# Kernel optimization log

Hardware: AMD Instinct MI355X
Metric: run time of the kernel (lower is better)

## Reference

```python
import jax, jax.numpy as jnp
import numpy as np

# ---- static config (matches init_kwargs) ----
N_NODES = 100_000; N_GRAPHS = 100; NPG = 1000; GRID = 32  # ceil(sqrt(1000))
N_EDGES = 1_600_000
IN_DIM = 64; POS_DIM = 16; HID = 16; HEADS = 4; HD = HID * HEADS  # 64
OUT_DIM = 10; DIV_WEIGHT = 0.1; BN_EPS = 1e-5; NEG_SLOPE = 0.2


def _segment_softmax(e, dst, n):
    emax = jax.ops.segment_max(e, dst, num_segments=n)
    p = jnp.exp(e - emax[dst])
    denom = jax.ops.segment_sum(p, dst, num_segments=n)
    return p / (denom[dst] + 1e-16)


def _gat(x, src, dst, n, W, a_src, a_dst, extra=None):
    """GATv1-style conv: per-head linear, additive attention, segment softmax over dst."""
    H, D = a_src.shape
    h = (x @ W).reshape(n, H, D)          # [N,H,D]
    s = (h * a_src).sum(-1)               # [N,H]
    d = (h * a_dst).sum(-1)               # [N,H]
    e = s[src] + d[dst]
    if extra is not None:
        e = e + extra                     # positional attention bias [E,H]
    e = jax.nn.leaky_relu(e, NEG_SLOPE)
    alpha = _segment_softmax(e, dst, n)   # [E,H]
    out = jax.ops.segment_sum(alpha[:, :, None] * h[src], dst, num_segments=n)
    return out.reshape(n, H * D)


def _div_loss(W):
    # head-diversity / orthogonality regularizer on per-head weight slices
    in_dim = W.shape[0]
    Wh = W.reshape(in_dim, HEADS, HID).transpose(1, 0, 2).reshape(HEADS, -1)
    Wn = Wh / (jnp.linalg.norm(Wh, axis=-1, keepdims=True) + 1e-12)
    G = Wn @ Wn.T
    off = G - jnp.eye(HEADS, dtype=W.dtype)
    return DIV_WEIGHT * (off ** 2).sum() / (HEADS * (HEADS - 1))


def _grid_pos(n, dtype):
    # normalized grid positions per graph (equal-size graphs of NPG nodes)
    i = jnp.arange(n) % NPG
    return jnp.stack([(i // GRID) / (GRID - 1), (i % GRID) / (GRID - 1)], -1).astype(dtype)


def _forward(x, edge_index, batch,
             pe_W, pe_b,
             l0_pW, l0_pas, l0_pad, l0_posW, l0_posb, l0_dW, l0_das, l0_dad, l0_fW, l0_fb, l0_g, l0_b,
             l1_pW, l1_pas, l1_pad, l1_posW, l1_posb, l1_dW, l1_das, l1_dad, l1_fW, l1_fb, l1_g, l1_b,
             res_W, res_b, task_W, task_b):
    n = x.shape[0]
    src, dst = edge_index[0], edge_index[1]
    pos = _grid_pos(n, x.dtype)
    rel = pos[dst] - pos[src]             # [E,2]
    h = jnp.concatenate([x, pos @ pe_W + pe_b], -1)  # positional encoding concat [N,80]

    def layer(h_in, pW, pas, pad, posW, posb, dW, das, dad, fW, fb, g, b):
        pos_out = _gat(h_in, src, dst, n, pW, pas, pad, extra=rel @ posW + posb)
        div_out = _gat(h_in, src, dst, n, dW, das, dad)
        fused = jnp.concatenate([pos_out, div_out], -1) @ fW + fb
        mu = fused.mean(0)
        var = fused.var(0)
        bn = (fused - mu) / jnp.sqrt(var + BN_EPS) * g + b
        return jax.nn.elu(bn), _div_loss(dW)

    h1, dl0 = layer(h, l0_pW, l0_pas, l0_pad, l0_posW, l0_posb, l0_dW, l0_das, l0_dad, l0_fW, l0_fb, l0_g, l0_b)
    h2, dl1 = layer(h1, l1_pW, l1_pas, l1_pad, l1_posW, l1_posb, l1_dW, l1_das, l1_dad, l1_fW, l1_fb, l1_g, l1_b)
    h2 = h2 + (h1 @ res_W + res_b)        # residual on layer >0

    pooled = jax.ops.segment_sum(h2, batch, num_segments=N_GRAPHS) / NPG  # mean pool
    task = pooled @ task_W + task_b       # [N_GRAPHS, OUT_DIM]
    return task, dl0 + dl1


def setup_inputs() -> dict:
    key = jax.random.key(0)
    keys = iter(jax.random.split(key, 64))
    nk = lambda: next(keys)
    w = lambda shape: jax.random.normal(nk(), shape, jnp.float32) * 0.05
    x = jax.random.normal(nk(), (N_NODES, IN_DIM), jnp.float32)
    gid = jnp.repeat(jnp.arange(N_GRAPHS), N_EDGES // N_GRAPHS)
    src = gid * NPG + jax.random.randint(nk(), (N_EDGES,), 0, NPG)
    dst = gid * NPG + jax.random.randint(nk(), (N_EDGES,), 0, NPG)
    edge_index = jnp.stack([src, dst]).astype(jnp.int32)
    batch = jnp.repeat(jnp.arange(N_GRAPHS), NPG).astype(jnp.int32)
    IN0 = IN_DIM + POS_DIM
    inp = dict(x=x, edge_index=edge_index, batch=batch,
               pe_W=w((2, POS_DIM)), pe_b=jnp.zeros((POS_DIM,), jnp.float32))
    for pref, din in (('l0', IN0), ('l1', HD)):
        inp[pref + '_pW'] = w((din, HD)); inp[pref + '_pas'] = w((HEADS, HID)); inp[pref + '_pad'] = w((HEADS, HID))
        inp[pref + '_posW'] = w((2, HEADS)); inp[pref + '_posb'] = jnp.zeros((HEADS,), jnp.float32)
        inp[pref + '_dW'] = w((din, HD)); inp[pref + '_das'] = w((HEADS, HID)); inp[pref + '_dad'] = w((HEADS, HID))
        inp[pref + '_fW'] = w((2 * HD, HD)); inp[pref + '_fb'] = jnp.zeros((HD,), jnp.float32)
        inp[pref + '_g'] = jnp.ones((HD,), jnp.float32); inp[pref + '_b'] = jnp.zeros((HD,), jnp.float32)
    inp['res_W'] = w((HD, HD)); inp['res_b'] = jnp.zeros((HD,), jnp.float32)
    inp['task_W'] = w((HD, OUT_DIM)); inp['task_b'] = jnp.zeros((OUT_DIM,), jnp.float32)
    return inp


def reference(x, edge_index, batch,
              pe_W, pe_b,
              l0_pW, l0_pas, l0_pad, l0_posW, l0_posb, l0_dW, l0_das, l0_dad, l0_fW, l0_fb, l0_g, l0_b,
              l1_pW, l1_pas, l1_pad, l1_posW, l1_posb, l1_dW, l1_das, l1_dad, l1_fW, l1_fb, l1_g, l1_b,
              res_W, res_b, task_W, task_b):
    return _forward(x, edge_index, batch, pe_W, pe_b,
                    l0_pW, l0_pas, l0_pad, l0_posW, l0_posb, l0_dW, l0_das, l0_dad, l0_fW, l0_fb, l0_g, l0_b,
                    l1_pW, l1_pas, l1_pad, l1_posW, l1_posb, l1_dW, l1_das, l1_dad, l1_fW, l1_fb, l1_g, l1_b,
                    res_W, res_b, task_W, task_b)
```

## Files before the change

### kernel.cpp

```cpp
#include <hip/hip_runtime.h>
#include <math.h>

#define N_NODES   100000
#define N_GRAPHS  100
#define NPG       1000
#define N_EDGES   1600000
#define EPG       16000
#define HID       16
#define HEADS     4
#define HD        64
#define OUT_DIM   10
#define BN_EPS    1e-5f
#define NEG_SLOPE 0.2f

#define LDA 68
#define GEMM_BLOCKS_C 1563

static const size_t OFF_SPART = 0;
static const size_t OFF_PEWS  = 7000000;
static const size_t OFF_STAT1 = 7001000;
static const size_t OFF_WFRAG = 7010000;
static const size_t OFF_WF2   = 7020000;
static const size_t OFF_POOL  = 7100000;
static const size_t OFF_HL    = 8000000;
static const size_t OFF_CAT   = 20800000;
static const size_t OFF_F0    = 33600000;
static const size_t OFF_F1    = 40000000;
static const size_t OFF_SPSP  = 46400000;
static const size_t OFF_SPSD  = 46800000;
static const size_t OFF_DPD   = 47200000;
static const size_t OFF_STATS = 48000000;
static const size_t OFF_CSR   = 48000128;
static const size_t OFF_SRT   = 48100144;

__device__ inline unsigned bf_pack(float x, float y) {
    unsigned ux = __float_as_uint(x);
    unsigned uy = __float_as_uint(y);
    ux = (ux + 0x7FFFu + ((ux >> 16) & 1u)) >> 16;
    uy = ((uy + 0x7FFFu + ((uy >> 16) & 1u)) >> 16) << 16;
    return ux | uy;
}
__device__ inline float bf_lo(unsigned u) { return __uint_as_float(u << 16); }
__device__ inline float bf_hi(unsigned u) { return __uint_as_float(u & 0xFFFF0000u); }

typedef __attribute__((ext_vector_type(8))) short bf16x8;
typedef __attribute__((ext_vector_type(4))) float f32x4;

__device__ inline bf16x8 frag_from(unsigned a, unsigned b, unsigned c, unsigned d) {
    uint4 u{a, b, c, d};
    return *reinterpret_cast<bf16x8*>(&u);
}

__global__ __launch_bounds__(1024) void sort_edges(const int* __restrict__ ei,
                                                   int* __restrict__ csr_off,
                                                   int* __restrict__ sorted_src) {
    __shared__ int hist[1024];
    __shared__ int scan[1024];
    const int g = blockIdx.x;
    const int t = threadIdx.x;
    const int* src = ei;
    const int* dst = ei + N_EDGES;
    const int e0 = g * EPG;
    const int nbase = g * NPG;

    hist[t] = 0;
    __syncthreads();
    for (int i = t; i < EPG; i += 1024) {
        int d = dst[e0 + i] - nbase;
        atomicAdd(&hist[d], 1);
    }
    __syncthreads();
    scan[t] = hist[t];
    __syncthreads();
    for (int off = 1; off < 1024; off <<= 1) {
        int v = (t >= off) ? scan[t - off] : 0;
        __syncthreads();
        scan[t] += v;
        __syncthreads();
    }
    int excl = scan[t] - hist[t];
    if (t < NPG) csr_off[nbase + t] = e0 + excl;
    if (g == 0 && t == 0) csr_off[N_NODES] = N_EDGES;
    __syncthreads();
    hist[t] = excl;
    __syncthreads();
    for (int i = t; i < EPG; i += 1024) {
        int s = src[e0 + i];
        int d = dst[e0 + i] - nbase;
        int slot = atomicAdd(&hist[d], 1);
        sorted_src[e0 + slot] = s;
    }
}

__global__ __launch_bounds__(256) void prep_all(const float* __restrict__ peW, const float* __restrict__ peb,
                                                const float* __restrict__ pW0, const float* __restrict__ dW0,
                                                const float* __restrict__ pW1, const float* __restrict__ dW1,
                                                const float* __restrict__ fW0, const float* __restrict__ fW1,
                                                float* __restrict__ pe,
                                                uint4* __restrict__ wfA,
                                                uint4* __restrict__ wfD,
                                                float* __restrict__ pool2,
                                                float* __restrict__ stats0,
                                                float* __restrict__ stats1) {
    const int t = threadIdx.x;
    const int b = blockIdx.x;
    if (b == 0) {
        if (t < 128) {
            int r = t >> 6, c = t & 63;
            float sp = 0.f, sd = 0.f;
            for (int m = 0; m < 16; ++m) {
                sp += peW[r * 16 + m] * pW0[(64 + m) * 64 + c];
                sd += peW[r * 16 + m] * dW0[(64 + m) * 64 + c];
            }
            pe[r * 64 + c] = sp;
            pe[192 + r * 64 + c] = sd;
        } else if (t < 192) {
            int c = t & 63;
            float sp = 0.f, sd = 0.f;
            for (int m = 0; m < 16; ++m) {
                sp += peb[m] * pW0[(64 + m) * 64 + c];
                sd += peb[m] * dW0[(64 + m) * 64 + c];
            }
            pe[128 + c] = sp;
            pe[320 + c] = sd;
        }
    } else if (b == 1) {
        for (int i = t; i < 2 * 4 * 4 * 64; i += 256) {
            const int lane  = i & 63;
            const int ct    = (i >> 6) & 3;
            const int kk    = (i >> 8) & 3;
            const int layer = i >> 10;
            const float* W = layer ? fW1 : fW0;
            const int col = ct * 16 + (lane & 15);
            const int kb  = kk * 32 + (lane >> 4) * 8;
            uint4 u;
            u.x = bf_pack(W[(kb + 0) * 64 + col], W[(kb + 1) * 64 + col]);
            u.y = bf_pack(W[(kb + 2) * 64 + col], W[(kb + 3) * 64 + col]);
            u.z = bf_pack(W[(kb + 4) * 64 + col], W[(kb + 5) * 64 + col]);
            u.w = bf_pack(W[(kb + 6) * 64 + col], W[(kb + 7) * 64 + col]);
            wfA[i] = u;
        }
    } else if (b == 2) {
        for (int i = t; i < 2048; i += 256) {
            const int lane  = i & 63;
            const int ct    = (i >> 6) & 3;
            const int kk    = (i >> 8) & 1;
            const int mat   = (i >> 9) & 1;
            const int layer = i >> 10;
            const float* W = layer ? (mat ? dW1 : pW1) : (mat ? dW0 : pW0);
            const int col = ct * 16 + (lane & 15);
            const int kb  = kk * 32 + (lane >> 4) * 8;
            uint4 u;
            u.x = bf_pack(W[(kb + 0) * 64 + col], W[(kb + 1) * 64 + col]);
            u.y = bf_pack(W[(kb + 2) * 64 + col], W[(kb + 3) * 64 + col]);
            u.z = bf_pack(W[(kb + 4) * 64 + col], W[(kb + 5) * 64 + col]);
            u.w = bf_pack(W[(kb + 6) * 64 + col], W[(kb + 7) * 64 + col]);
            wfD[i] = u;
        }
    } else {
        for (int i = t; i < 2 * N_GRAPHS * 64; i += 256) pool2[i] = 0.f;
        if (t < 128) { stats0[t] = 0.f; stats1[t] = 0.f; }
    }
}

__global__ __launch_bounds__(128) void reduce_stats(const float* __restrict__ part,
                                                    float* __restrict__ stats) {
    const int c = threadIdx.x;
    const int nb = GEMM_BLOCKS_C;
    const int per = (nb + gridDim.x - 1) / gridDim.x;
    const int b0 = blockIdx.x * per;
    int b1 = b0 + per; if (b1 > nb) b1 = nb;
    float s = 0.f;
    for (int b = b0; b < b1; ++b) s += part[(size_t)b * 128 + c];
    atomicAdd(&stats[c], s);
}

template <bool PE, bool BN>
__global__ __launch_bounds__(256) void gemm_dual_mfma(const float* __restrict__ A,
                                                      const unsigned* __restrict__ wf2,
                                                      const float* __restrict__ pe,
                                                      const float* __restrict__ pas,
                                                      const float* __restrict__ pad_,
                                                      const float* __restrict__ das,
                                                      const float* __restrict__ dad,
                                                      const float* __restrict__ posW,
                                                      const float* __restrict__ posb,
                                                      const float* __restrict__ stats,
                                                      const float* __restrict__ gamma,
                                                      const float* __restrict__ beta,
                                                      float* __restrict__ poolF,
                                                      unsigned* __restrict__ hl,
                                                      float* __restrict__ sps_p,
                                                      float* __restrict__ sps_d,
                                                      float2* __restrict__ dpd) {
    __shared__ float sD[4 * 2 * 16 * LDA];
    const int t = threadIdx.x;
    const int w = t >> 6, lane = t & 63;
    const int cidx = lane & 15, khi = lane >> 4;
    const int node0 = blockIdx.x * 64;

    bf16x8 wf[2][2][4];
#pragma unroll
    for (int mat = 0; mat < 2; ++mat)
#pragma unroll
        for (int kk = 0; kk < 2; ++kk)
#pragma unroll
            for (int ct = 0; ct < 4; ++ct)
                wf[mat][kk][ct] = *reinterpret_cast<const bf16x8*>(
                    wf2 + (size_t)((((mat * 2 + kk) * 4 + ct) * 64) + lane) * 4);

    const int node0w = node0 + w * 16;
    int gn = node0w + cidx; if (gn > N_NODES - 1) gn = N_NODES - 1;
    const float* ar = A + (size_t)gn * 64;
    bf16x8 ah[2], al[2];
#pragma unroll
    for (int kk = 0; kk < 2; ++kk) {
        const int k0 = kk * 32 + khi * 8;
        float4 f0 = *reinterpret_cast<const float4*>(ar + k0);
        float4 f1 = *reinterpret_cast<const float4*>(ar + k0 + 4);
        if (BN) {
            const float invN = 1.0f / (float)N_NODES;
            float4 sa = *reinterpret_cast<const float4*>(&stats[k0]);
            float4 sb = *reinterpret_cast<const float4*>(&stats[k0 + 4]);
            float4 qa = *reinterpret_cast<const float4*>(&stats[64 + k0]);
            float4 qb = *reinterpret_cast<const float4*>(&stats[64 + k0 + 4]);
            float4 ga = *reinterpret_cast<const float4*>(&gamma[k0]);
            float4 gb = *reinterpret_cast<const float4*>(&gamma[k0 + 4]);
            float4 ba = *reinterpret_cast<const float4*>(&beta[k0]);
            float4 bb = *reinterpret_cast<const float4*>(&beta[k0 + 4]);
            float sc[8], sh[8];
            float ss[8] = {sa.x, sa.y, sa.z, sa.w, sb.x, sb.y, sb.z, sb.w};
            float qq[8] = {qa.x, qa.y, qa.z, qa.w, qb.x, qb.y, qb.z, qb.w};
            float gg[8] = {ga.x, ga.y, ga.z, ga.w, gb.x, gb.y, gb.z, gb.w};
            float bt[8] = {ba.x, ba.y, ba.z, ba.w, bb.x, bb.y, bb.z, bb.w};
#pragma unroll
            for (int i = 0; i < 8; ++i) {
                float mu = ss[i] * invN;
                float var = qq[i] * invN - mu * mu;
                float iv = rsqrtf(var + BN_EPS);
                sc[i] = iv * gg[i];
                sh[i] = bt[i] - mu * sc[i];
            }
            auto ap = [&](float v, int i) {
                float r = fmaf(v, sc[i], sh[i]);
                return r > 0.f ? r : (__expf(r) - 1.f);
            };
            f0.x = ap(f0.x, 0); f0.y = ap(f0.y, 1); f0.z = ap(f0.z, 2); f0.w = ap(f0.w, 3);
            f1.x = ap(f1.x, 4); f1.y = ap(f1.y, 5); f1.z = ap(f1.z, 6); f1.w = ap(f1.w, 7);
            if (node0w < N_NODES) {
                const int node_l = node0w + cidx;
                const bool okn = node_l < N_NODES;
                const int gl = node_l / NPG;
                const int g0 = node0w / NPG;
                int lastn = node0w + 15; if (lastn > N_NODES - 1) lastn = N_NODES - 1;
                const int g1 = lastn / NPG;
                float p8[8] = {f0.x, f0.y, f0.z, f0.w, f1.x, f1.y, f1.z, f1.w};
                {
                    const bool m = okn && (gl == g0);
#pragma unroll
                    for (int i = 0; i < 8; ++i) {
                        float tv = m ? p8[i] : 0.f;
                        tv += __shfl_xor(tv, 1); tv += __shfl_xor(tv, 2);
                        tv += __shfl_xor(tv, 4); tv += __shfl_xor(tv, 8);
                        if (cidx == 0) atomicAdd(&poolF[g0 * 64 + k0 + i], tv);
                    }
                }
                if (g1 != g0) {
                    const bool m = okn && (gl == g1);
#pragma unroll
                    for (int i = 0; i < 8; ++i) {
                        float tv = m ? p8[i] : 0.f;
                        tv += __shfl_xor(tv, 1); tv += __shfl_xor(tv, 2);
                        tv += __shfl_xor(tv, 4); tv += __shfl_xor(tv, 8);
                        if (cidx == 0) atomicAdd(&poolF[g1 * 64 + k0 + i], tv);
                    }
                }
            }
        }
        unsigned h0 = bf_pack(f0.x, f0.y), h1 = bf_pack(f0.z, f0.w);
        unsigned h2 = bf_pack(f1.x, f1.y), h3 = bf_pack(f1.z, f1.w);
        unsigned l0 = bf_pack(f0.x - bf_lo(h0), f0.y - bf_hi(h0));
        unsigned l1 = bf_pack(f0.z - bf_lo(h1), f0.w - bf_hi(h1));
        unsigned l2 = bf_pack(f1.x - bf_lo(h2), f1.y - bf_hi(h2));
        unsigned l3 = bf_pack(f1.z - bf_lo(h3), f1.w - bf_hi(h3));
        ah[kk] = frag_from(h0, h1, h2, h3);
        al[kk] = frag_from(l0, l1, l2, l3);
    }

    f32x4 ap4[4], ad4[4];
#pragma unroll
    for (int ct = 0; ct < 4; ++ct) { ap4[ct] = 0.f; ad4[ct] = 0.f; }
#pragma unroll
    for (int ct = 0; ct < 4; ++ct) {
        ap4[ct] = __builtin_amdgcn_mfma_f32_16x16x32_bf16(ah[0], wf[0][0][ct], ap4[ct], 0, 0, 0);
        ap4[ct] = __builtin_amdgcn_mfma_f32_16x16x32_bf16(ah[1], wf[0][1][ct], ap4[ct], 0, 0, 0);
        ap4[ct] = __builtin_amdgcn_mfma_f32_16x16x32_bf16(al[0], wf[0][0][ct], ap4[ct], 0, 0, 0);
        ap4[ct] = __builtin_amdgcn_mfma_f32_16x16x32_bf16(al[1], wf[0][1][ct], ap4[ct], 0, 0, 0);
        ad4[ct] = __builtin_amdgcn_mfma_f32_16x16x32_bf16(ah[0], wf[1][0][ct], ad4[ct], 0, 0, 0);
        ad4[ct] = __builtin_amdgcn_mfma_f32_16x16x32_bf16(ah[1], wf[1][1][ct], ad4[ct], 0, 0, 0);
        ad4[ct] = __builtin_amdgcn_mfma_f32_16x16x32_bf16(al[0], wf[1][0][ct], ad4[ct], 0, 0, 0);
        ad4[ct] = __builtin_amdgcn_mfma_f32_16x16x32_bf16(al[1], wf[1][1][ct], ad4[ct], 0, 0, 0);
    }

    {
        float* base = sD + w * (2 * 16 * LDA);
#pragma unroll
        for (int ct = 0; ct < 4; ++ct)
#pragma unroll
            for (int q = 0; q < 4; ++q) {
                base[(khi * 4 + q) * LDA + ct * 16 + cidx]                 = ap4[ct][q];
                base[16 * LDA + (khi * 4 + q) * LDA + ct * 16 + cidx]      = ad4[ct][q];
            }
    }
    __syncthreads();

    const int tx = t & 15, ty = t >> 4;
    const int c4 = tx * 4;
    float4 accp[4], accd[4];
#pragma unroll
    for (int j = 0; j < 4; ++j) {
        const int n = ty * 4 + j;
        const float* bp = sD + (n >> 4) * (2 * 16 * LDA) + (n & 15) * LDA;
        accp[j] = *reinterpret_cast<const float4*>(bp + c4);
        accd[j] = *reinterpret_cast<const float4*>(bp + 16 * LDA + c4);
    }

    if (PE) {
        float4 pp0 = *reinterpret_cast<const float4*>(&pe[c4]);
        float4 pp1 = *reinterpret_cast<const float4*>(&pe[64 + c4]);
        float4 ppb = *reinterpret_cast<const float4*>(&pe[128 + c4]);
        float4 pd0 = *reinterpret_cast<const float4*>(&pe[192 + c4]);
        float4 pd1 = *reinterpret_cast<const float4*>(&pe[256 + c4]);
        float4 pdb = *reinterpret_cast<const float4*>(&pe[320 + c4]);
#pragma unroll
        for (int j = 0; j < 4; ++j) {
            int node = node0 + ty * 4 + j;
            int r = node % NPG;
            float px = (float)(r >> 5) * (1.0f / 31.0f);
            float py = (float)(r & 31) * (1.0f / 31.0f);
            accp[j].x += px * pp0.x + py * pp1.x + ppb.x;
            accp[j].y += px * pp0.y + py * pp1.y + ppb.y;
            accp[j].z += px * pp0.z + py * pp1.z + ppb.z;
            accp[j].w += px * pp0.w + py * pp1.w + ppb.w;
            accd[j].x += px * pd0.x + py * pd1.x + pdb.x;
            accd[j].y += px * pd0.y + py * pd1.y + pdb.y;
            accd[j].z += px * pd0.z + py * pd1.z + pdb.z;
            accd[j].w += px * pd0.w + py * pd1.w + pdb.w;
        }
    }

    float4 pasv = *reinterpret_cast<const float4*>(&pas[c4]);
    float4 padv = *reinterpret_cast<const float4*>(&pad_[c4]);
    float4 dasv = *reinterpret_cast<const float4*>(&das[c4]);
    float4 dadv = *reinterpret_cast<const float4*>(&dad[c4]);
    const int h = tx >> 2;
    const float pw0 = posW[h], pw1 = posW[4 + h], pb = posb[h];
    const int cu = tx * 2;
#pragma unroll
    for (int j = 0; j < 4; ++j) {
        const int node = node0 + ty * 4 + j;
        float vps = accp[j].x * pasv.x + accp[j].y * pasv.y + accp[j].z * pasv.z + accp[j].w * pasv.w;
        float vpd = accp[j].x * padv.x + accp[j].y * padv.y + accp[j].z * padv.z + accp[j].w * padv.w;
        float vds = accd[j].x * dasv.x + accd[j].y * dasv.y + accd[j].z * dasv.z + accd[j].w * dasv.w;
        float vdd = accd[j].x * dadv.x + accd[j].y * dadv.y + accd[j].z * dadv.z + accd[j].w * dadv.w;
        vps += __shfl_xor(vps, 1); vps += __shfl_xor(vps, 2);
        vpd += __shfl_xor(vpd, 1); vpd += __shfl_xor(vpd, 2);
        vds += __shfl_xor(vds, 1); vds += __shfl_xor(vds, 2);
        vdd += __shfl_xor(vdd, 1); vdd += __shfl_xor(vdd, 2);
        if (node < N_NODES) {
            uint2 up, ud;
            up.x = bf_pack(accp[j].x, accp[j].y); up.y = bf_pack(accp[j].z, accp[j].w);
            ud.x = bf_pack(accd[j].x, accd[j].y); ud.y = bf_pack(accd[j].z, accd[j].w);
            *reinterpret_cast<uint2*>(&hl[(size_t)node * 64 + cu])      = up;
            *reinterpret_cast<uint2*>(&hl[(size_t)node * 64 + 32 + cu]) = ud;
            if ((tx & 3) == 0) {
                const int r = node % NPG;
                const float pxn = (float)(r >> 5) * (1.0f / 31.0f);
                const float pyn = (float)(r & 31) * (1.0f / 31.0f);
                const float posdot = pxn * pw0 + pyn * pw1;
                sps_p[node * 4 + h] = vps - posdot;
                sps_d[node * 4 + h] = vds;
                dpd[node * 4 + h] = float2{vpd + posdot + pb, vdd};
            }
        }
    }
}

__global__ __launch_bounds__(256) void gemm_mfma_bf(const unsigned* __restrict__ A,
                                                    const unsigned* __restrict__ wfrag,
                                                    const float* __restrict__ bias,
                                                    float* __restrict__ out,
                                                    float* __restrict__ spart) {
    __shared__ float red[512];
    const int t = threadIdx.x;
    const int lane = t & 63;
    const int cidx = lane & 15;
    const int khi  = lane >> 4;

    bf16x8 wf[4][4];
#pragma unroll
    for (int kk = 0; kk < 4; ++kk)
#pragma unroll
        for (int ct = 0; ct < 4; ++ct)
            wf[kk][ct] = *reinterpret_cast<const bf16x8*>(wfrag + (size_t)((kk * 4 + ct) * 64 + lane) * 4);

    float bias_r[4];
#pragma unroll
    for (int ct = 0; ct < 4; ++ct) bias_r[ct] = bias[ct * 16 + cidx];

    float ls[4] = {0.f, 0.f, 0.f, 0.f};
    float lq[4] = {0.f, 0.f, 0.f, 0.f};

    const int NW  = gridDim.x << 2;
    const int wid = (blockIdx.x << 2) + (t >> 6);
    for (int tile = wid; tile < N_NODES / 16; tile += NW) {
        const int node0 = tile << 4;
        const unsigned* arow = A + (size_t)(node0 + cidx) * 64 + khi * 4;
        bf16x8 a0 = *reinterpret_cast<const bf16x8*>(arow);
        bf16x8 a1 = *reinterpret_cast<const bf16x8*>(arow + 16);
        bf16x8 a2 = *reinterpret_cast<const bf16x8*>(arow + 32);
        bf16x8 a3 = *reinterpret_cast<const bf16x8*>(arow + 48);

        f32x4 acc[4];
#pragma unroll
        for (int ct = 0; ct < 4; ++ct) acc[ct] = 0.f;
#pragma unroll
        for (int ct = 0; ct < 4; ++ct) {
            acc[ct] = __builtin_amdgcn_mfma_f32_16x16x32_bf16(a0, wf[0][ct], acc[ct], 0, 0, 0);
            acc[ct] = __builtin_amdgcn_mfma_f32_16x16x32_bf16(a1, wf[1][ct], acc[ct], 0, 0, 0);
            acc[ct] = __builtin_amdgcn_mfma_f32_16x16x32_bf16(a2, wf[2][ct], acc[ct], 0, 0, 0);
            acc[ct] = __builtin_amdgcn_mfma_f32_16x16x32_bf16(a3, wf[3][ct], acc[ct], 0, 0, 0);
        }

        const int nbase = node0 + (khi << 2);
#pragma unroll
        for (int ct = 0; ct < 4; ++ct) {
#pragma unroll
            for (int q = 0; q < 4; ++q) {
                float v = acc[ct][q] + bias_r[ct];
                out[(size_t)(nbase + q) * 64 + ct * 16 + cidx] = v;
                ls[ct] += v;
                lq[ct] = fmaf(v, v, lq[ct]);
            }
        }
    }

#pragma unroll
    for (int ct = 0; ct < 4; ++ct) {
        ls[ct] += __shfl_xor(ls[ct], 16); ls[ct] += __shfl_xor(ls[ct], 32);
        lq[ct] += __shfl_xor(lq[ct], 16); lq[ct] += __shfl_xor(lq[ct], 32);
    }
    if (lane < 16) {
        const int w = t >> 6;
#pragma unroll
        for (int ct = 0; ct < 4; ++ct) {
            red[w * 64 + ct * 16 + lane]       = ls[ct];
            red[256 + w * 64 + ct * 16 + lane] = lq[ct];
        }
    }
    __syncthreads();
    if (t < 64) {
        float s  = red[t] + red[64 + t] + red[128 + t] + red[192 + t];
        float sq = red[256 + t] + red[320 + t] + red[384 + t] + red[448 + t];
        spart[(size_t)blockIdx.x * 128 + t]      = s;
        spart[(size_t)blockIdx.x * 128 + 64 + t] = sq;
    }
}

__global__ __launch_bounds__(256) void gat_fused(const unsigned* __restrict__ hl,
                                                 const float* __restrict__ sps_p,
                                                 const float* __restrict__ sps_d,
                                                 const float2* __restrict__ dpd,
                                                 const int* __restrict__ csr_off,
                                                 const int* __restrict__ sorted_src,
                                                 unsigned* __restrict__ gat_cat) {
    const int b = blockIdx.x;
    const int logical = (b & 7) * 3125 + (b >> 3);
    const int v = logical * 4 + (threadIdx.x >> 6);
    if (v >= N_NODES) return;
    const int lane = threadIdx.x & 63;
    const int j1 = lane >> 3;
    const int p1 = (lane >> 2) & 1;
    const int h1 = lane & 3;
    const int phneed = ((lane >> 5) << 2) | ((lane & 31) >> 3);

    const float* __restrict__ spl = p1 ? sps_d : sps_p;
    const float2 dv1 = dpd[(size_t)v * 4 + h1];
    const float dval1 = p1 ? dv1.y : dv1.x;

    const int beg = __builtin_amdgcn_readfirstlane(csr_off[v]);
    const int end = __builtin_amdgcn_readfirstlane(csr_off[v + 1]);

    float2 acc = {0.f, 0.f};
    float wpart = 0.f;
    int e = beg;
    const int nfull = (end - beg) >> 3;

    int sA = 0, sB = 0;
    float svA = 0.f, svB = 0.f;
    if (nfull >= 1) { sA = sorted_src[e + j1]; svA = spl[(size_t)sA * 4 + h1]; }
    if (nfull >= 2) { sB = sorted_src[e + 8 + j1]; }

    for (int k = 0; k < nfull; ++k, e += 8) {
        int sC = 0;
        if (k + 2 < nfull) sC = sorted_src[e + 16 + j1];
        if (k + 1 < nfull) svB = spl[(size_t)sB * 4 + h1];
        float elog = svA + dval1;
        elog = fmaxf(elog, NEG_SLOPE * elog);
        float w = __expf(elog);
        wpart += w;
#pragma unroll
        for (int jj = 0; jj < 8; ++jj) {
            int sj = __builtin_amdgcn_readlane(sA, jj * 8);
            float wj = __shfl(w, jj * 8 + phneed);
            unsigned u = hl[((size_t)sj << 6) + lane];
            acc.x = fmaf(wj, bf_lo(u), acc.x);
            acc.y = fmaf(wj, bf_hi(u), acc.y);
        }
        sA = sB; sB = sC; svA = svB;
    }

    if (e < end) {
        const int nj = end - e;
        int ee = e + j1; if (ee >= end) ee = end - 1;
        int s = sorted_src[ee];
        float sval = spl[(size_t)s * 4 + h1];
        float elog = sval + dval1;
        elog = fmaxf(elog, NEG_SLOPE * elog);
        float w = __expf(elog);
        if (j1 >= nj) w = 0.f;
        wpart += w;
        for (int jj = 0; jj < nj; ++jj) {
            int sj = __builtin_amdgcn_readlane(s, jj * 8);
            float wj = __shfl(w, jj * 8 + phneed);
            unsigned u = hl[((size_t)sj << 6) + lane];
            acc.x = fmaf(wj, bf_lo(u), acc.x);
            acc.y = fmaf(wj, bf_hi(u), acc.y);
        }
    }
    wpart += __shfl_xor(wpart, 8);
    wpart += __shfl_xor(wpart, 16);
    wpart += __shfl_xor(wpart, 32);
    const float wsum = __shfl(wpart, phneed);
    const float inv = 1.0f / (wsum + 1e-16f);
    gat_cat[(size_t)v * 64 + lane] = bf_pack(acc.x * inv, acc.y * inv);
}

template <bool WRITEF>
__global__ __launch_bounds__(256) void bn_elu(float* __restrict__ F, const float* __restrict__ stats,
                                              const float* __restrict__ gamma, const float* __restrict__ beta,
                                              float* __restrict__ pooled) {
    __shared__ float red[256];
    const int t = threadIdx.x;
    const int idx = blockIdx.x * 256 + t;
    const int c = t & 63;
    float mu = stats[c] * (1.0f / (float)N_NODES);
    float var = stats[64 + c] * (1.0f / (float)N_NODES) - mu * mu;
    float inv = rsqrtf(var + BN_EPS);
    float v = (F[idx] - mu) * inv * gamma[c] + beta[c];
    v = (v > 0.f) ? v : expm1f(v);
    if (WRITEF) F[idx] = v;
    red[t] = v;
    __syncthreads();
    if (t < 64) {
        float s = red[c] + red[64 + c] + red[128 + c] + red[192 + c];
        int g = (blockIdx.x * 4) / NPG;
        atomicAdd(&pooled[g * 64 + c], s);
    }
}

__global__ __launch_bounds__(64) void task_head(const float* __restrict__ pooled,
                                                const float* __restrict__ pooledF0,
                                                const float* __restrict__ resW,
                                                const float* __restrict__ resb,
                                                const float* __restrict__ taskW,
                                                const float* __restrict__ taskb,
                                                float* __restrict__ out) {
    const int g = blockIdx.x;
    const int c = threadIdx.x;
    float rc = 0.f;
    const float* pf = pooledF0 + g * 64;
    for (int k = 0; k < 64; ++k)
        rc = fmaf(pf[k], resW[k * 64 + c], rc);
    float p = (pooled[g * 64 + c] + rc) * (1.0f / (float)NPG) + resb[c];
#pragma unroll
    for (int o = 0; o < OUT_DIM; ++o) {
        float partial = p * taskW[c * OUT_DIM + o];
#pragma unroll
        for (int m = 1; m < 64; m <<= 1) partial += __shfl_xor(partial, m);
        if (c == 0) out[g * OUT_DIM + o] = partial + taskb[o];
    }
}

__global__ __launch_bounds__(256) void div_loss(const float* __restrict__ dW0,
                                                const float* __restrict__ dW1,
                                                float* __restrict__ out) {
    __shared__ float red[16][16];
    float total = 0.f;
    for (int layer = 0; layer < 2; ++layer) {
        const float* W = layer ? dW1 : dW0;
        const int din = layer ? 64 : 80;
        const int p = threadIdx.x & 15;
        const int s16 = threadIdx.x >> 4;
        const int i = p >> 2, j = p & 3;
        float acc = 0.f;
        const int Kk = din * 16;
        for (int kk = s16; kk < Kk; kk += 16) {
            int rrow = kk >> 4, cc = kk & 15;
            acc += W[rrow * 64 + i * 16 + cc] * W[rrow * 64 + j * 16 + cc];
        }
        red[p][s16] = acc;
        __syncthreads();
        if (threadIdx.x < 16) {
            float s = 0.f;
            for (int m = 0; m < 16; ++m) s += red[threadIdx.x][m];
            red[threadIdx.x][0] = s;
        }
        __syncthreads();
        if (threadIdx.x == 0) {
            float G[4][4], nrm[4];
            for (int a = 0; a < 4; ++a)
                for (int b = 0; b < 4; ++b) G[a][b] = red[a * 4 + b][0];
            for (int a = 0; a < 4; ++a) nrm[a] = sqrtf(G[a][a]) + 1e-12f;
            float l = 0.f;
            for (int a = 0; a < 4; ++a)
                for (int b = 0; b < 4; ++b) {
                    float gn = G[a][b] / (nrm[a] * nrm[b]);
                    float off = gn - (a == b ? 1.f : 0.f);
                    l += off * off;
                }
            total += 0.1f * l / 12.f;
        }
        __syncthreads();
    }
    if (threadIdx.x == 0) *out = total;
}

extern "C" void kernel_launch(void* const* d_in, const int* in_sizes, int n_in,
                              void* d_out, int out_size, void* d_ws, size_t ws_size,
                              hipStream_t stream) {
    const float* x      = (const float*)d_in[0];
    const int*   ei     = (const int*)d_in[1];
    const float* peW    = (const float*)d_in[3];
    const float* peb    = (const float*)d_in[4];

    const float* l_pW[2]   = {(const float*)d_in[5],  (const float*)d_in[17]};
    const float* l_pas[2]  = {(const float*)d_in[6],  (const float*)d_in[18]};
    const float* l_pad[2]  = {(const float*)d_in[7],  (const float*)d_in[19]};
    const float* l_posW[2] = {(const float*)d_in[8],  (const float*)d_in[20]};
    const float* l_posb[2] = {(const float*)d_in[9],  (const float*)d_in[21]};
    const float* l_dW[2]   = {(const float*)d_in[10], (const float*)d_in[22]};
    const float* l_das[2]  = {(const float*)d_in[11], (const float*)d_in[23]};
    const float* l_dad[2]  = {(const float*)d_in[12], (const float*)d_in[24]};
    const float* l_fW[2]   = {(const float*)d_in[13], (const float*)d_in[25]};
    const float* l_fb[2]   = {(const float*)d_in[14], (const float*)d_in[26]};
    const float* l_g[2]    = {(const float*)d_in[15], (const float*)d_in[27]};
    const float* l_b[2]    = {(const float*)d_in[16], (const float*)d_in[28]};
    const float* res_W  = (const float*)d_in[29];
    const float* res_b  = (const float*)d_in[30];
    const float* task_W = (const float*)d_in[31];
    const float* task_b = (const float*)d_in[32];

    float* ws = (float*)d_ws;
    float* spart   = ws + OFF_SPART;
    float* pe_ws   = ws + OFF_PEWS;
    float* stats1  = ws + OFF_STAT1;
    float* wfrag   = ws + OFF_WFRAG;
    float* wfrag2  = ws + OFF_WF2;
    float* pooled  = ws + OFF_POOL;
    float* pooledF0= ws + OFF_POOL + 6400;
    unsigned* hl   = (unsigned*)(ws + OFF_HL);
    unsigned* cat_bf = (unsigned*)(ws + OFF_CAT);
    float* F0      = ws + OFF_F0;
    float* F1      = ws + OFF_F1;
    float* sps_p   = ws + OFF_SPSP;
    float* sps_d   = ws + OFF_SPSD;
    float2* dpd    = (float2*)(ws + OFF_DPD);
    float* stats0  = ws + OFF_STATS;
    int*   csr_off    = (int*)(ws + OFF_CSR);
    int*   sorted_src = (int*)(ws + OFF_SRT);
    float* out = (float*)d_out;

    const int NODE_BLOCKS = (N_NODES + 3) / 4;
    const int GEMM_BLOCKS = GEMM_BLOCKS_C;
    const int MFMA_BLOCKS = GEMM_BLOCKS_C;
    const int BN_BLOCKS   = N_NODES * 64 / 256;

    sort_edges<<<N_GRAPHS, 1024, 0, stream>>>(ei, csr_off, sorted_src);
    prep_all<<<4, 256, 0, stream>>>(peW, peb, l_pW[0], l_dW[0], l_pW[1], l_dW[1],
                                    l_fW[0], l_fW[1], pe_ws,
                                    (uint4*)wfrag, (uint4*)wfrag2,
                                    pooled, stats0, stats1);

    gemm_dual_mfma<true, false><<<GEMM_BLOCKS, 256, 0, stream>>>(x, (const unsigned*)wfrag2, pe_ws,
        l_pas[0], l_pad[0], l_das[0], l_dad[0], l_posW[0], l_posb[0],
        stats0, l_g[0], l_b[0], pooledF0,
        hl, sps_p, sps_d, dpd);
    gat_fused<<<NODE_BLOCKS, 256, 0, stream>>>(hl, sps_p, sps_d, dpd, csr_off, sorted_src, cat_bf);
    gemm_mfma_bf<<<MFMA_BLOCKS, 256, 0, stream>>>(cat_bf, (const unsigned*)wfrag,
                                                  l_fb[0], F0, spart);
    reduce_stats<<<16, 128, 0, stream>>>(spart, stats0);

    gemm_dual_mfma<false, true><<<GEMM_BLOCKS, 256, 0, stream>>>(F0, (const unsigned*)wfrag2 + 4096, pe_ws,
        l_pas[1], l_pad[1], l_das[1], l_dad[1], l_posW[1], l_posb[1],
        stats0, l_g[0], l_b[0], pooledF0,
        hl, sps_p, sps_d, dpd);
    gat_fused<<<NODE_BLOCKS, 256, 0, stream>>>(hl, sps_p, sps_d, dpd, csr_off, sorted_src, cat_bf);
    gemm_mfma_bf<<<MFMA_BLOCKS, 256, 0, stream>>>(cat_bf, (const unsigned*)wfrag + 4096,
                                                  l_fb[1], F1, spart);
    reduce_stats<<<16, 128, 0, stream>>>(spart, stats1);
    bn_elu<false><<<BN_BLOCKS, 256, 0, stream>>>(F1, stats1, l_g[1], l_b[1], pooled);

    task_head<<<N_GRAPHS, 64, 0, stream>>>(pooled, pooledF0, res_W, res_b,
                                           task_W, task_b, out);
    div_loss<<<1, 256, 0, stream>>>(l_dW[0], l_dW[1], out + 1000);
}
```

Before: 467.6 us.

## Fuse GAT aggregation with the output MFMA GEMM through shared memory

The GAT edge aggregation and the following bf16 MFMA linear layer are merged into one kernel. Each block aggregates 16 nodes (4 per wave) into a shared-memory tile and then multiplies that tile by the weight fragments directly. This removes the global write and re-read of the concatenated bf16 intermediate and one kernel launch per layer. In exchange, each wave handles 4 nodes serially, which gives less latency hiding per wave. The GEMM_BLOCKS constant also changes from 1563 to 1563 (same value), and the number of partial-stat blocks rises to 6250, making the stats reduction larger.

```diff
diff --git a/kernel.cpp b/kernel.cpp
--- a/kernel.cpp
+++ b/kernel.cpp
@@ -14,7 +14,7 @@
 #define NEG_SLOPE 0.2f
 
 #define LDA 68
-#define GEMM_BLOCKS_C 1563
+#define GG_BLOCKS 6250
 
 static const size_t OFF_SPART = 0;
 static const size_t OFF_PEWS  = 7000000;
@@ -23,7 +23,6 @@
 static const size_t OFF_WF2   = 7020000;
 static const size_t OFF_POOL  = 7100000;
 static const size_t OFF_HL    = 8000000;
-static const size_t OFF_CAT   = 20800000;
 static const size_t OFF_F0    = 33600000;
 static const size_t OFF_F1    = 40000000;
 static const size_t OFF_SPSP  = 46400000;
@@ -164,9 +163,8 @@
 }
 
 __global__ __launch_bounds__(128) void reduce_stats(const float* __restrict__ part,
-                                                    float* __restrict__ stats) {
+                                                    float* __restrict__ stats, int nb) {
     const int c = threadIdx.x;
-    const int nb = GEMM_BLOCKS_C;
     const int per = (nb + gridDim.x - 1) / gridDim.x;
     const int b0 = blockIdx.x * per;
     int b1 = b0 + per; if (b1 > nb) b1 = nb;
@@ -386,164 +384,123 @@
     }
 }
 
-__global__ __launch_bounds__(256) void gemm_mfma_bf(const unsigned* __restrict__ A,
-                                                    const unsigned* __restrict__ wfrag,
-                                                    const float* __restrict__ bias,
-                                                    float* __restrict__ out,
-                                                    float* __restrict__ spart) {
-    __shared__ float red[512];
+__global__ __launch_bounds__(256) void gat_gemm(const unsigned* __restrict__ hl,
+                                                const float* __restrict__ sps_p,
+                                                const float* __restrict__ sps_d,
+                                                const float2* __restrict__ dpd,
+                                                const int* __restrict__ csr_off,
+                                                const int* __restrict__ sorted_src,
+                                                const unsigned* __restrict__ wfrag,
+                                                const float* __restrict__ bias,
+                                                float* __restrict__ outF,
+                                                float* __restrict__ spart) {
+    __shared__ unsigned sCat[16 * LDA];
     const int t = threadIdx.x;
-    const int lane = t & 63;
-    const int cidx = lane & 15;
-    const int khi  = lane >> 4;
-
-    bf16x8 wf[4][4];
-#pragma unroll
-    for (int kk = 0; kk < 4; ++kk)
-#pragma unroll
-        for (int ct = 0; ct < 4; ++ct)
-            wf[kk][ct] = *reinterpret_cast<const bf16x8*>(wfrag + (size_t)((kk * 4 + ct) * 64 + lane) * 4);
-
-    float bias_r[4];
-#pragma unroll
-    for (int ct = 0; ct < 4; ++ct) bias_r[ct] = bias[ct * 16 + cidx];
-
-    float ls[4] = {0.f, 0.f, 0.f, 0.f};
-    float lq[4] = {0.f, 0.f, 0.f, 0.f};
-
-    const int NW  = gridDim.x << 2;
-    const int wid = (blockIdx.x << 2) + (t >> 6);
-    for (int tile = wid; tile < N_NODES / 16; tile += NW) {
-        const int node0 = tile << 4;
-        const unsigned* arow = A + (size_t)(node0 + cidx) * 64 + khi * 4;
-        bf16x8 a0 = *reinterpret_cast<const bf16x8*>(arow);
-        bf16x8 a1 = *reinterpret_cast<const bf16x8*>(arow + 16);
-        bf16x8 a2 = *reinterpret_cast<const bf16x8*>(arow + 32);
-        bf16x8 a3 = *reinterpret_cast<const bf16x8*>(arow + 48);
-
-        f32x4 acc[4];
-#pragma unroll
-        for (int ct = 0; ct < 4; ++ct) acc[ct] = 0.f;
-#pragma unroll
-        for (int ct = 0; ct < 4; ++ct) {
-            acc[ct] = __builtin_amdgcn_mfma_f32_16x16x32_bf16(a0, wf[0][ct], acc[ct], 0, 0, 0);
-            acc[ct] = __builtin_amdgcn_mfma_f32_16x16x32_bf16(a1, wf[1][ct], acc[ct], 0, 0, 0);
-            acc[ct] = __builtin_amdgcn_mfma_f32_16x16x32_bf16(a2, wf[2][ct], acc[ct], 0, 0, 0);
-            acc[ct] = __builtin_amdgcn_mfma_f32_16x16x32_bf16(a3, wf[3][ct], acc[ct], 0, 0, 0);
-        }
-
-        const int nbase = node0 + (khi << 2);
-#pragma unroll
-        for (int ct = 0; ct < 4; ++ct) {
-#pragma unroll
-            for (int q = 0; q < 4; ++q) {
-                float v = acc[ct][q] + bias_r[ct];
-                out[(size_t)(nbase + q) * 64 + ct * 16 + cidx] = v;
-                ls[ct] += v;
-                lq[ct] = fmaf(v, v, lq[ct]);
-            }
-        }
-    }
-
-#pragma unroll
-    for (int ct = 0; ct < 4; ++ct) {
-        ls[ct] += __shfl_xor(ls[ct], 16); ls[ct] += __shfl_xor(ls[ct], 32);
-        lq[ct] += __shfl_xor(lq[ct], 16); lq[ct] += __shfl_xor(lq[ct], 32);
-    }
-    if (lane < 16) {
-        const int w = t >> 6;
-#pragma unroll
-        for (int ct = 0; ct < 4; ++ct) {
-            red[w * 64 + ct * 16 + lane]       = ls[ct];
-            red[256 + w * 64 + ct * 16 + lane] = lq[ct];
-        }
-    }
-    __syncthreads();
-    if (t < 64) {
-        float s  = red[t] + red[64 + t] + red[128 + t] + red[192 + t];
-        float sq = red[256 + t] + red[320 + t] + red[384 + t] + red[448 + t];
-        spart[(size_t)blockIdx.x * 128 + t]      = s;
-        spart[(size_t)blockIdx.x * 128 + 64 + t] = sq;
-    }
-}
-
-__global__ __launch_bounds__(256) void gat_fused(const unsigned* __restrict__ hl,
-                                                 const float* __restrict__ sps_p,
-                                                 const float* __restrict__ sps_d,
-                                                 const float2* __restrict__ dpd,
-                                                 const int* __restrict__ csr_off,
-                                                 const int* __restrict__ sorted_src,
-                                                 unsigned* __restrict__ gat_cat) {
-    const int b = blockIdx.x;
-    const int logical = (b & 7) * 3125 + (b >> 3);
-    const int v = logical * 4 + (threadIdx.x >> 6);
-    if (v >= N_NODES) return;
-    const int lane = threadIdx.x & 63;
+    const int w = t >> 6, lane = t & 63;
+
+    const int orig = blockIdx.x;
+    const int xcd = orig & 7;
+    const int qq = GG_BLOCKS >> 3, rr = GG_BLOCKS & 7;
+    const int lb = (xcd < rr ? xcd * (qq + 1) : rr * (qq + 1) + (xcd - rr) * qq) + (orig >> 3);
+    const int node0 = lb * 16;
+
     const int j1 = lane >> 3;
     const int p1 = (lane >> 2) & 1;
     const int h1 = lane & 3;
     const int phneed = ((lane >> 5) << 2) | ((lane & 31) >> 3);
-
     const float* __restrict__ spl = p1 ? sps_d : sps_p;
-    const float2 dv1 = dpd[(size_t)v * 4 + h1];
-    const float dval1 = p1 ? dv1.y : dv1.x;
-
-    const int beg = __builtin_amdgcn_readfirstlane(csr_off[v]);
-    const int end = __builtin_amdgcn_readfirstlane(csr_off[v + 1]);
-
-    float2 acc = {0.f, 0.f};
-    float wpart = 0.f;
-    int e = beg;
-    const int nfull = (end - beg) >> 3;
-
-    int sA = 0, sB = 0;
-    float svA = 0.f, svB = 0.f;
-    if (nfull >= 1) { sA = sorted_src[e + j1]; svA = spl[(size_t)sA * 4 + h1]; }
-    if (nfull >= 2) { sB = sorted_src[e + 8 + j1]; }
-
-    for (int k = 0; k < nfull; ++k, e += 8) {
-        int sC = 0;
-        if (k + 2 < nfull) sC = sorted_src[e + 16 + j1];
-        if (k + 1 < nfull) svB = spl[(size_t)sB * 4 + h1];
-        float elog = svA + dval1;
-        elog = fmaxf(elog, NEG_SLOPE * elog);
-        float w = __expf(elog);
-        wpart += w;
-#pragma unroll
-        for (int jj = 0; jj < 8; ++jj) {
-            int sj = __builtin_amdgcn_readlane(sA, jj * 8);
-            float wj = __shfl(w, jj * 8 + phneed);
-            unsigned u = hl[((size_t)sj << 6) + lane];
-            acc.x = fmaf(wj, bf_lo(u), acc.x);
-            acc.y = fmaf(wj, bf_hi(u), acc.y);
-        }
-        sA = sB; sB = sC; svA = svB;
-    }
-
-    if (e < end) {
-        const int nj = end - e;
-        int ee = e + j1; if (ee >= end) ee = end - 1;
-        int s = sorted_src[ee];
-        float sval = spl[(size_t)s * 4 + h1];
-        float elog = sval + dval1;
-        elog = fmaxf(elog, NEG_SLOPE * elog);
-        float w = __expf(elog);
-        if (j1 >= nj) w = 0.f;
-        wpart += w;
-        for (int jj = 0; jj < nj; ++jj) {
-            int sj = __builtin_amdgcn_readlane(s, jj * 8);
-            float wj = __shfl(w, jj * 8 + phneed);
-            unsigned u = hl[((size_t)sj << 6) + lane];
-            acc.x = fmaf(wj, bf_lo(u), acc.x);
-            acc.y = fmaf(wj, bf_hi(u), acc.y);
-        }
-    }
-    wpart += __shfl_xor(wpart, 8);
-    wpart += __shfl_xor(wpart, 16);
-    wpart += __shfl_xor(wpart, 32);
-    const float wsum = __shfl(wpart, phneed);
-    const float inv = 1.0f / (wsum + 1e-16f);
-    gat_cat[(size_t)v * 64 + lane] = bf_pack(acc.x * inv, acc.y * inv);
+
+    for (int i = 0; i < 4; ++i) {
+        const int v = node0 + w * 4 + i;
+        const float2 dv1 = dpd[(size_t)v * 4 + h1];
+        const float dval1 = p1 ? dv1.y : dv1.x;
+        const int beg = __builtin_amdgcn_readfirstlane(csr_off[v]);
+        const int end = __builtin_amdgcn_readfirstlane(csr_off[v + 1]);
+
+        float2 acc = {0.f, 0.f};
+        float wpart = 0.f;
+        int e = beg;
+        const int nfull = (end - beg) >> 3;
+
+        int sA = 0, sB = 0;
+        float svA = 0.f, svB = 0.f;
+        if (nfull >= 1) { sA = sorted_src[e + j1]; svA = spl[(size_t)sA * 4 + h1]; }
+        if (nfull >= 2) { sB = sorted_src[e + 8 + j1]; }
+
+        for (int k = 0; k < nfull; ++k, e += 8) {
+            int sC = 0;
+            if (k + 2 < nfull) sC = sorted_src[e + 16 + j1];
+            if (k + 1 < nfull) svB = spl[(size_t)sB * 4 + h1];
+            float elog = svA + dval1;
+            elog = fmaxf(elog, NEG_SLOPE * elog);
+            float wv = __expf(elog);
+            wpart += wv;
+#pragma unroll
+            for (int jj = 0; jj < 8; ++jj) {
+                int sj = __builtin_amdgcn_readlane(sA, jj * 8);
+                float wj = __shfl(wv, jj * 8 + phneed);
+                unsigned u = hl[((size_t)sj << 6) + lane];
+                acc.x = fmaf(wj, bf_lo(u), acc.x);
+                acc.y = fmaf(wj, bf_hi(u), acc.y);
+            }
+            sA = sB; sB = sC; svA = svB;
+        }
+
+        if (e < end) {
+            const int nj = end - e;
+            int ee = e + j1; if (ee >= end) ee = end - 1;
+            int s = sorted_src[ee];
+            float sval = spl[(size_t)s * 4 + h1];
+            float elog = sval + dval1;
+            elog = fmaxf(elog, NEG_SLOPE * elog);
+            float wv = __expf(elog);
+            if (j1 >= nj) wv = 0.f;
+            wpart += wv;
+            for (int jj = 0; jj < nj; ++jj) {
+                int sj = __builtin_amdgcn_readlane(s, jj * 8);
+                float wj = __shfl(wv, jj * 8 + phneed);
+                unsigned u = hl[((size_t)sj << 6) + lane];
+                acc.x = fmaf(wj, bf_lo(u), acc.x);
+                acc.y = fmaf(wj, bf_hi(u), acc.y);
+            }
+        }
+        wpart += __shfl_xor(wpart, 8);
+        wpart += __shfl_xor(wpart, 16);
+        wpart += __shfl_xor(wpart, 32);
+        const float wsum = __shfl(wpart, phneed);
+        const float inv = 1.0f / (wsum + 1e-16f);
+        sCat[(w * 4 + i) * LDA + lane] = bf_pack(acc.x * inv, acc.y * inv);
+    }
+    __syncthreads();
+
+    const int cidx = lane & 15, khi = lane >> 4;
+    bf16x8 wfr[4];
+#pragma unroll
+    for (int kk = 0; kk < 4; ++kk)
+        wfr[kk] = *reinterpret_cast<const bf16x8*>(wfrag + (size_t)((kk * 4 + w) * 64 + lane) * 4);
+    const float biasv = bias[w * 16 + cidx];
+
+    f32x4 acc4 = 0.f;
+#pragma unroll
+    for (int kk = 0; kk < 4; ++kk) {
+        bf16x8 a = *reinterpret_cast<const bf16x8*>(&sCat[cidx * LDA + kk * 16 + khi * 4]);
+        acc4 = __builtin_amdgcn_mfma_f32_16x16x32_bf16(a, wfr[kk], acc4, 0, 0, 0);
+    }
+
+    float ls = 0.f, lq = 0.f;
+#pragma unroll
+    for (int q = 0; q < 4; ++q) {
+        float v = acc4[q] + biasv;
+        outF[(size_t)(node0 + khi * 4 + q) * 64 + w * 16 + cidx] = v;
+        ls += v;
+        lq = fmaf(v, v, lq);
+    }
+    ls += __shfl_xor(ls, 16); ls += __shfl_xor(ls, 32);
+    lq += __shfl_xor(lq, 16); lq += __shfl_xor(lq, 32);
+    if (khi == 0) {
+        spart[(size_t)lb * 128 + w * 16 + cidx]      = ls;
+        spart[(size_t)lb * 128 + 64 + w * 16 + cidx] = lq;
+    }
 }
 
 template <bool WRITEF>
@@ -670,7 +627,6 @@
     float* pooled  = ws + OFF_POOL;
     float* pooledF0= ws + OFF_POOL + 6400;
     unsigned* hl   = (unsigned*)(ws + OFF_HL);
-    unsigned* cat_bf = (unsigned*)(ws + OFF_CAT);
     float* F0      = ws + OFF_F0;
     float* F1      = ws + OFF_F1;
     float* sps_p   = ws + OFF_SPSP;
@@ -681,9 +637,7 @@
     int*   sorted_src = (int*)(ws + OFF_SRT);
     float* out = (float*)d_out;
 
-    const int NODE_BLOCKS = (N_NODES + 3) / 4;
-    const int GEMM_BLOCKS = GEMM_BLOCKS_C;
-    const int MFMA_BLOCKS = GEMM_BLOCKS_C;
+    const int GEMM_BLOCKS = (N_NODES + 63) / 64;
     const int BN_BLOCKS   = N_NODES * 64 / 256;
 
     sort_edges<<<N_GRAPHS, 1024, 0, stream>>>(ei, csr_off, sorted_src);
@@ -696,19 +650,17 @@
         l_pas[0], l_pad[0], l_das[0], l_dad[0], l_posW[0], l_posb[0],
         stats0, l_g[0], l_b[0], pooledF0,
         hl, sps_p, sps_d, dpd);
-    gat_fused<<<NODE_BLOCKS, 256, 0, stream>>>(hl, sps_p, sps_d, dpd, csr_off, sorted_src, cat_bf);
-    gemm_mfma_bf<<<MFMA_BLOCKS, 256, 0, stream>>>(cat_bf, (const unsigned*)wfrag,
-                                                  l_fb[0], F0, spart);
-    reduce_stats<<<16, 128, 0, stream>>>(spart, stats0);
+    gat_gemm<<<GG_BLOCKS, 256, 0, stream>>>(hl, sps_p, sps_d, dpd, csr_off, sorted_src,
+        (const unsigned*)wfrag, l_fb[0], F0, spart);
+    reduce_stats<<<32, 128, 0, stream>>>(spart, stats0, GG_BLOCKS);
 
     gemm_dual_mfma<false, true><<<GEMM_BLOCKS, 256, 0, stream>>>(F0, (const unsigned*)wfrag2 + 4096, pe_ws,
         l_pas[1], l_pad[1], l_das[1], l_dad[1], l_posW[1], l_posb[1],
         stats0, l_g[0], l_b[0], pooledF0,
         hl, sps_p, sps_d, dpd);
-    gat_fused<<<NODE_BLOCKS, 256, 0, stream>>>(hl, sps_p, sps_d, dpd, csr_off, sorted_src, cat_bf);
-    gemm_mfma_bf<<<MFMA_BLOCKS, 256, 0, stream>>>(cat_bf, (const unsigned*)wfrag + 4096,
-                                                  l_fb[1], F1, spart);
-    reduce_stats<<<16, 128, 0, stream>>>(spart, stats1);
+    gat_gemm<<<GG_BLOCKS, 256, 0, stream>>>(hl, sps_p, sps_d, dpd, csr_off, sorted_src,
+        (const unsigned*)wfrag + 4096, l_fb[1], F1, spart);
+    reduce_stats<<<32, 128, 0, stream>>>(spart, stats1, GG_BLOCKS);
     bn_elu<false><<<BN_BLOCKS, 256, 0, stream>>>(F1, stats1, l_g[1], l_b[1], pooled);
 
     task_head<<<N_GRAPHS, 64, 0, stream>>>(pooled, pooledF0, res_W, res_b,
```

Measured after the change: 501.1 us. 7.2% more time.
